# Kernel optimization log

Hardware: AMD Instinct MI355X
Metric: run time of the kernel (lower is better)

The kernel has to match this reference:

```python
import jax, jax.numpy as jnp
import numpy as np

TEMP = 5.0          # temperature_attn
BN_EPS = 1e-5
L2_EPS = 1e-8

def _conv2d(x, w):
    # x: [N,C,H,W], w: [O,C,3,3], SAME padding, stride 1
    return jax.lax.conv_general_dilated(x, w, (1, 1), 'SAME',
                                        dimension_numbers=('NCHW', 'OIHW', 'NCHW'))

def _conv_over_base(x, w):
    # separable 4D conv piece: 2D conv over the (Hb,Wb) pair of the 6D tensor
    BN, C, Hm, Wm, Hb, Wb = x.shape
    O = w.shape[0]
    y = _conv2d(x.transpose(0, 2, 3, 1, 4, 5).reshape(BN * Hm * Wm, C, Hb, Wb), w)
    return y.reshape(BN, Hm, Wm, O, Hb, Wb).transpose(0, 3, 1, 2, 4, 5)

def _conv_over_mem(x, w):
    # separable 4D conv piece: 2D conv over the (Hm,Wm) pair of the 6D tensor
    BN, C, Hm, Wm, Hb, Wb = x.shape
    O = w.shape[0]
    y = _conv2d(x.transpose(0, 4, 5, 1, 2, 3).reshape(BN * Hb * Wb, C, Hm, Wm), w)
    return y.reshape(BN, Hb, Wb, O, Hm, Wm).transpose(0, 3, 4, 5, 1, 2)

def _l2norm(x, axis):
    n = jnp.sqrt(jnp.sum(x * x, axis=axis, keepdims=True))
    return x / jnp.maximum(n, L2_EPS)

def _gaussian_normalize(x, axis):
    m = jnp.mean(x, axis=axis, keepdims=True)
    v = jnp.var(x, axis=axis, ddof=1, keepdims=True)  # torch.var is unbiased
    return (x - m) / jnp.sqrt(v + BN_EPS)

def setup_inputs() -> dict:
    key = jax.random.key(0)
    ks = jax.random.split(key, 10)
    B, N, C, H = 8, 64, 512, 10
    R, HID, NCLS = 64, 16, 100
    f32 = jnp.float32
    return {
        'feat_b': jax.random.normal(ks[0], (B, C, H, H), f32),
        'feat_m': jax.random.normal(ks[1], (N, C, H, H), f32),
        'w1x1':  jax.random.normal(ks[2], (R, C), f32) * 0.05,     # cca_1x1 conv weight
        'bn_gamma': jnp.ones((R,), f32),
        'bn_beta':  jnp.zeros((R,), f32),
        'w1a': jax.random.normal(ks[3], (HID, 1, 3, 3), f32) * 0.3,   # CCA block1, base-pair conv
        'w1b': jax.random.normal(ks[4], (HID, HID, 3, 3), f32) * 0.1, # CCA block1, mem-pair conv
        'w2a': jax.random.normal(ks[5], (1, HID, 3, 3), f32) * 0.1,   # CCA block2, base-pair conv
        'w2b': jax.random.normal(ks[6], (1, 1, 3, 3), f32) * 0.3,     # CCA block2, mem-pair conv
        'w_fc': jax.random.normal(ks[7], (NCLS, 2 * C), f32) * 0.02,  # memory-wrap head
        'b_fc': jnp.zeros((NCLS,), f32),
    }

def reference(feat_b, feat_m, w1x1, bn_gamma, bn_beta, w1a, w1b, w2a, w2b, w_fc, b_fc):
    B, C, Hb, Wb = feat_b.shape
    N, _, Hm, Wm = feat_m.shape
    # channel mean shift
    fb_s = feat_b - feat_b.mean(axis=1, keepdims=True)
    fm_s = feat_m - feat_m.mean(axis=1, keepdims=True)
    # 1x1 conv + BatchNorm(eval: mu=0,var=1) + ReLU, then L2-normalize over channels
    def proj(x):
        y = jnp.einsum('bchw,rc->brhw', x, w1x1)
        y = jax.nn.relu(y * bn_gamma[None, :, None, None] + bn_beta[None, :, None, None])
        return _l2norm(y, axis=1)
    fbp, fmp = proj(fb_s), proj(fm_s)
    # 6D cross-correlation map [B,N,Hm,Wm,Hb,Wb]
    corr = jnp.einsum('bchw,ncij->bnijhw', fbp, fmp)
    # CCA module: two separable 4D conv blocks (1->16, ReLU, 16->1)
    x = corr.reshape(B * N, 1, Hm, Wm, Hb, Wb)
    h = jax.nn.relu(_conv_over_mem(_conv_over_base(x, w1a), w1b))
    corr = _conv_over_mem(_conv_over_base(h, w2a), w2b).reshape(B, N, Hm, Wm, Hb, Wb)
    # memory-direction normalize+softmax (over Hm*Wm)
    cm = corr.reshape(B, N, Hm * Wm, Hb, Wb)
    cm = jax.nn.softmax(_gaussian_normalize(cm, 2) / TEMP, axis=2)
    attn_memory = cm.reshape(B, N, Hm, Wm, Hb, Wb).sum(axis=(4, 5))  # [B,N,Hm,Wm]
    # batch-direction normalize+softmax (over Hb*Wb)
    cb = corr.reshape(B, N, Hm, Wm, Hb * Wb)
    cb = jax.nn.softmax(_gaussian_normalize(cb, 4) / TEMP, axis=4)
    attn_batch = cb.reshape(B, N, Hm, Wm, Hb, Wb).sum(axis=(2, 3))  # [B,N,Hb,Wb] (used only for extras)
    # per-input attended memory embedding [B,N,C]
    att_mem = jnp.einsum('bnhw,nchw->bnc', attn_memory, feat_m) / (Hm * Wm)
    # memory wrap: cosine content weights over N + linear head on [enc ; mem_vec]
    enc = feat_b.mean(axis=(2, 3))                       # [B,C]
    enc_n = _l2norm(enc, axis=1)
    mem_n = _l2norm(att_mem, axis=2)
    w = jax.nn.softmax(jnp.einsum('bc,bnc->bn', enc_n, mem_n), axis=1)
    mem_vec = jnp.einsum('bn,bnc->bc', w, att_mem)
    logits = jnp.concatenate([enc, mem_vec], axis=1) @ w_fc.T + b_fc
    return logits
```

## Files before the change

### kernel.cpp

```cpp
#include <hip/hip_runtime.h>
#include <hip/hip_bf16.h>


__global__ __launch_bounds__(512) void k_proj2(const float* __restrict__ feat_b,
                                               const float* __restrict__ feat_m,
                                               const float* __restrict__ w1x1,
                                               const float* __restrict__ gamma,
                                               const float* __restrict__ beta,
                                               float* __restrict__ fbp,
                                               float* __restrict__ fmp) {
    __shared__ __align__(16) float xt[64][104];
    __shared__ __align__(16) float wt[64][68];
    __shared__ float colsum[100];
    __shared__ float wsumL[64];
    __shared__ float invL[100];
    const int tid = threadIdx.x;
    const int img = blockIdx.x;
    const float* x;
    float* outp;
    if (img < 8) { x = feat_b + (size_t)img * 51200; outp = fbp + (size_t)img * 6400; }
    else         { x = feat_m + (size_t)(img - 8) * 51200; outp = fmp + (size_t)(img - 8) * 6400; }

    if (tid < 100) colsum[tid] = 0.f;
    if (tid < 64) wsumL[tid] = 0.f;
    const int r = tid >> 3, q = tid & 7;
    float acc[13];
#pragma unroll
    for (int j = 0; j < 13; ++j) acc[j] = 0.f;
    __syncthreads();

    for (int ct = 0; ct < 8; ++ct) {
        for (int i = tid; i < 1600; i += 512) {
            int row = i / 25, c4 = (i % 25) * 4;
            *(float4*)&xt[row][c4] = *(const float4*)&x[(size_t)(ct * 64 + row) * 100 + c4];
        }
        for (int i = tid; i < 1024; i += 512) {
            int row = i / 16, c4 = (i % 16) * 4;
            *(float4*)&wt[row][c4] = *(const float4*)&w1x1[(size_t)row * 512 + ct * 64 + c4];
        }
        __syncthreads();
        if (tid < 100) {
            float s = 0.f;
            for (int c = 0; c < 64; ++c) s += xt[c][tid];
            colsum[tid] += s;
        }
        if (tid < 64) {
            float s = 0.f;
            for (int c = 0; c < 64; ++c) s += wt[tid][c];
            wsumL[tid] += s;
        }
        for (int c = 0; c < 64; ++c) {
            float w = wt[r][c];
#pragma unroll
            for (int j = 0; j < 13; ++j) {
                int hw = q + 8 * j;
                if (hw < 100) acc[j] = fmaf(w, xt[c][hw], acc[j]);
            }
        }
        __syncthreads();
    }
    float g = gamma[r], be = beta[r], wsr = wsumL[r];
#pragma unroll
    for (int j = 0; j < 13; ++j) {
        int hw = q + 8 * j;
        if (hw < 100) {
            float mean = colsum[hw] * (1.f / 512.f);
            xt[r][hw] = fmaxf((acc[j] - mean * wsr) * g + be, 0.f);
        }
    }
    __syncthreads();
    if (tid < 100) {
        float ss = 0.f;
        for (int rr = 0; rr < 64; ++rr) { float z = xt[rr][tid]; ss = fmaf(z, z, ss); }
        invL[tid] = 1.f / fmaxf(sqrtf(ss), 1e-8f);
    }
    __syncthreads();
    for (int i = tid; i < 6400; i += 512) {
        int rr = i / 100, hw = i % 100;
        outp[i] = xt[rr][hw] * invL[hw];
    }
}

__global__ __launch_bounds__(512) void k_corr(const float* __restrict__ fbp,
                                              const float* __restrict__ fmp,
                                              const float* __restrict__ w1a,
                                              const float* __restrict__ w1b,
                                              float* __restrict__ K1w,
                                              float* __restrict__ corr) {
    if (blockIdx.x == 512) {
        for (int t = threadIdx.x; t < 432; t += 512) {
            int tap = t >> 4, c = t & 15;
            int dm = tap / 3, dbh = tap % 3;
            float g0 = 0.f, g1 = 0.f, g2 = 0.f;
            for (int cp = 0; cp < 16; ++cp) {
                float wb = w1b[(c * 16 + cp) * 9 + dm];
                g0 = fmaf(wb, w1a[cp * 9 + dbh * 3 + 0], g0);
                g1 = fmaf(wb, w1a[cp * 9 + dbh * 3 + 1], g1);
                g2 = fmaf(wb, w1a[cp * 9 + dbh * 3 + 2], g2);
            }
            int base = tap * 64 + c;
            K1w[base]      = g0;
            K1w[base + 16] = 0.5f * (g0 + g1 + g2);
            K1w[base + 32] = 0.5f * (g0 - g1 + g2);
            K1w[base + 48] = g2;
        }
        return;
    }
    __shared__ __align__(16) float A[6400];
    __shared__ __align__(16) float B[6400];
    const int tid = threadIdx.x, bn = blockIdx.x;
    const float* fm = fmp + (size_t)(bn & 63) * 6400;
    const float* fb = fbp + (size_t)(bn >> 6) * 6400;
    for (int i = tid * 4; i < 6400; i += 2048) {
        *(float4*)&A[i] = *(const float4*)&fm[i];
        *(float4*)&B[i] = *(const float4*)&fb[i];
    }
    __syncthreads();
    float* dst = corr + (size_t)bn * 10000;
    for (int u = tid; u < 625; u += 512) {
        int m0 = (u / 25) * 4, b0 = (u % 25) * 4;
        float acc[4][4] = {};
        for (int r = 0; r < 64; ++r) {
            float4 av = *(const float4*)&A[r * 100 + m0];
            float4 bv = *(const float4*)&B[r * 100 + b0];
            float a[4] = {av.x, av.y, av.z, av.w};
            float bb[4] = {bv.x, bv.y, bv.z, bv.w};
#pragma unroll
            for (int i = 0; i < 4; ++i)
#pragma unroll
                for (int j = 0; j < 4; ++j) acc[i][j] = fmaf(a[i], bb[j], acc[i][j]);
        }
#pragma unroll
        for (int i = 0; i < 4; ++i)
#pragma unroll
            for (int j = 0; j < 4; ++j) dst[(m0 + i) * 100 + (b0 + j)] = acc[i][j];
    }
}

__global__ __launch_bounds__(64, 4) void k_cca(const float* __restrict__ corr,
                                               const float* __restrict__ K1w,
                                               const float* __restrict__ w2a,
                                               float* __restrict__ g1out) {
    __shared__ float ring[2184];
    const int lane = threadIdx.x;
    const int wm = blockIdx.x, bn = blockIdx.y;
    const int mr_lo = blockIdx.z * 5, mr_hi = mr_lo + 4;
    const int R_max = (mr_hi + 1 < 9) ? mr_hi + 1 : 9;
    const int u = lane < 50 ? lane : 49;
    const int bh = u / 5, p = u % 5, bw0 = 2 * p;
    const bool act = lane < 50;

    for (int i = lane; i < 2184; i += 64) ring[i] = 0.f;
    const float* cbase = corr + (size_t)bn * 10000 + (wm - 1) * 100;
    const int i0 = (wm == 0) ? 100 : 0;
    const int i1 = (wm == 9) ? 200 : 300;

    auto prefetch = [&](int R) {
        if (R < 0 || R > R_max) return;
        const float* src = cbase + R * 1000;
        float* dslot = &ring[(R & 3) * 504];
#pragma unroll
        for (int k = 0; k < 5; ++k) {
            int i = lane + k * 64;
            if (i >= i0 && i < i1) {
                int mc = i / 100, t = i % 100;
                dslot[mc * 168 + (t / 10 + 1) * 14 + (t % 10 + 1)] = src[i];
            }
        }
    };
    prefetch(mr_lo - 1);
    prefetch(mr_lo);
    prefetch(mr_lo + 1);

    const int rbase = bh * 14 + bw0;
    for (int mr = mr_lo; mr <= mr_hi; ++mr) {
        prefetch(mr + 2);

        float A1[16], A2[16], A3[16], A4[16];
#pragma unroll
        for (int c = 0; c < 16; ++c) { A1[c] = 0.f; A2[c] = 0.f; A3[c] = 0.f; A4[c] = 0.f; }
        for (int dmh = 0; dmh < 3; ++dmh) {
            int mrow = mr + dmh - 1;
            if ((unsigned)mrow >= 10u) continue;
            const float* slab0 = &ring[(mrow & 3) * 504];
#pragma unroll
            for (int dmw = 0; dmw < 3; ++dmw) {
                bool mv = (unsigned)(wm + dmw - 1) < 10u;
                const float* cb = (mv ? slab0 + dmw * 168 : &ring[2016]) + rbase;
                const float* kp = K1w + (dmh * 3 + dmw) * 192;
#pragma unroll
                for (int dbh = 0; dbh < 3; ++dbh) {
                    float2 lo = *(const float2*)&cb[dbh * 14];
                    float2 hi = *(const float2*)&cb[dbh * 14 + 2];
                    float t1 = lo.x - hi.x;
                    float t2 = lo.y + hi.x;
                    float t3 = hi.x - lo.y;
                    float t4 = lo.y - hi.y;
                    const float* kq = kp + dbh * 64;
#pragma unroll
                    for (int c = 0; c < 16; ++c) {
                        A1[c] = fmaf(t1, kq[c], A1[c]);
                        A2[c] = fmaf(t2, kq[16 + c], A2[c]);
                        A3[c] = fmaf(t3, kq[32 + c], A3[c]);
                        A4[c] = fmaf(t4, kq[48 + c], A4[c]);
                    }
                }
            }
        }

        float P00 = 0.f, P01 = 0.f, P10 = 0.f, P11 = 0.f, P20 = 0.f, P21 = 0.f;
#pragma unroll
        for (int c = 0; c < 16; ++c) {
            float r0 = fmaxf(A1[c] + A2[c] + A3[c], 0.f);
            float r1 = fmaxf(A2[c] - A3[c] - A4[c], 0.f);
            float lA = __shfl(r1, lane - 1); lA = (p > 0) ? lA : 0.f;
            float rA = __shfl(r0, lane + 1); rA = (p < 4) ? rA : 0.f;
            const float* wq = w2a + c * 9;
            P00 = fmaf(wq[0], lA, fmaf(wq[1], r0, fmaf(wq[2], r1, P00)));
            P01 = fmaf(wq[0], r0, fmaf(wq[1], r1, fmaf(wq[2], rA, P01)));
            P10 = fmaf(wq[3], lA, fmaf(wq[4], r0, fmaf(wq[5], r1, P10)));
            P11 = fmaf(wq[3], r0, fmaf(wq[4], r1, fmaf(wq[5], rA, P11)));
            P20 = fmaf(wq[6], lA, fmaf(wq[7], r0, fmaf(wq[8], r1, P20)));
            P21 = fmaf(wq[6], r0, fmaf(wq[7], r1, fmaf(wq[8], rA, P21)));
        }
        float u00 = __shfl(P00, lane - 5), u01 = __shfl(P01, lane - 5);
        float u20 = __shfl(P20, lane + 5), u21 = __shfl(P21, lane + 5);
        if (bh == 0) { u00 = 0.f; u01 = 0.f; }
        if (bh == 9) { u20 = 0.f; u21 = 0.f; }
        float g0 = P10 + u00 + u20;
        float g1v = P11 + u01 + u21;
        if (act) {
            float2 st; st.x = g0; st.y = g1v;
            *(float2*)&g1out[(size_t)bn * 10000 + (mr * 10 + wm) * 100 + bh * 10 + bw0] = st;
        }
    }
}

__global__ __launch_bounds__(512) void k_msoft2(const float* __restrict__ g1,
                                                const float* __restrict__ w2b,
                                                float* __restrict__ attnm) {
    __shared__ float gt[10000];
    const int tid = threadIdx.x, bn = blockIdx.x;
    const float* src = g1 + (size_t)bn * 10000;
    for (int i = tid; i < 10000; i += 512) gt[i] = src[i];
    __syncthreads();
    float wb[9];
#pragma unroll
    for (int t = 0; t < 9; ++t) wb[t] = w2b[t];
    const int b = tid >> 2, q = tid & 3;
    const bool act = tid < 400;
    float ev[25];
    float se = 0.f;
    if (act) {
        float s = 0.f, ss = 0.f;
#pragma unroll
        for (int i = 0; i < 25; ++i) {
            int m = q * 25 + i, mh = m / 10, mw = m % 10;
            float v = 0.f;
#pragma unroll
            for (int dh = 0; dh < 3; ++dh) {
                int rr = mh + dh - 1;
                if ((unsigned)rr < 10u) {
#pragma unroll
                    for (int dw = 0; dw < 3; ++dw) {
                        int ww = mw + dw - 1;
                        if ((unsigned)ww < 10u)
                            v = fmaf(wb[dh * 3 + dw], gt[(rr * 10 + ww) * 100 + b], v);
                    }
                }
            }
            ev[i] = v;
            s += v; ss = fmaf(v, v, ss);
        }
        s += __shfl_xor(s, 1); s += __shfl_xor(s, 2);
        ss += __shfl_xor(ss, 1); ss += __shfl_xor(ss, 2);
        float mean = s * 0.01f;
        float var = (ss - 100.f * mean * mean) * (1.f / 99.f);
        float istd = 0.2f / sqrtf(var + 1e-5f);
        float mx = -1e30f;
#pragma unroll
        for (int i = 0; i < 25; ++i) mx = fmaxf(mx, ev[i]);
        mx = fmaxf(mx, __shfl_xor(mx, 1)); mx = fmaxf(mx, __shfl_xor(mx, 2));
#pragma unroll
        for (int i = 0; i < 25; ++i) {
            float e = expf((ev[i] - mx) * istd);
            ev[i] = e; se += e;
        }
        se += __shfl_xor(se, 1); se += __shfl_xor(se, 2);
    }
    __syncthreads();
    if (act) {
        float inv = 1.f / se;
#pragma unroll
        for (int i = 0; i < 25; ++i) gt[(q * 25 + i) * 100 + b] = ev[i] * inv;
    }
    __syncthreads();
    if (act) {
        int m = tid >> 2;
        float s2 = 0.f;
#pragma unroll
        for (int i = 0; i < 25; ++i) s2 += gt[m * 100 + q * 25 + i];
        s2 += __shfl_xor(s2, 1); s2 += __shfl_xor(s2, 2);
        if (q == 0) attnm[bn * 100 + m] = s2;
    }
}

__global__ __launch_bounds__(128) void k_attmem(const float* __restrict__ attnm,
                                                const float* __restrict__ feat_m,
                                                float* __restrict__ attm) {
    __shared__ float A[8][100];
    int n = blockIdx.x, cq = blockIdx.y, tid = threadIdx.x;
    for (int i = tid; i < 800; i += 128) {
        int b = i / 100, m = i % 100;
        A[b][m] = attnm[(b * 64 + n) * 100 + m];
    }
    __syncthreads();
    int c = cq * 128 + tid;
    const float* fp = feat_m + ((size_t)n * 512 + c) * 100;
    float acc[8] = {};
    for (int m4 = 0; m4 < 100; m4 += 4) {
        float4 v = *(const float4*)&fp[m4];
#pragma unroll
        for (int b = 0; b < 8; ++b) {
            acc[b] = fmaf(A[b][m4], v.x, acc[b]);
            acc[b] = fmaf(A[b][m4 + 1], v.y, acc[b]);
            acc[b] = fmaf(A[b][m4 + 2], v.z, acc[b]);
            acc[b] = fmaf(A[b][m4 + 3], v.w, acc[b]);
        }
    }
#pragma unroll
    for (int b = 0; b < 8; ++b)
        attm[((size_t)(b * 64 + n)) * 512 + c] = acc[b] * 0.01f;
}

__global__ __launch_bounds__(512) void k_final(const float* __restrict__ feat_b,
                                               const float* __restrict__ attm,
                                               const float* __restrict__ w_fc,
                                               const float* __restrict__ b_fc,
                                               float* __restrict__ out) {
    __shared__ float attL[64 * 513];
    __shared__ float encL[512];
    __shared__ float mv[512];
    __shared__ float wL[64];
    __shared__ float red[512];
    int b = blockIdx.x, tid = threadIdx.x;
    {
        const float* fp = feat_b + ((size_t)b * 512 + tid) * 100;
        float s = 0.f;
        for (int m = 0; m < 100; m += 4) {
            float4 v = *(const float4*)&fp[m];
            s += v.x + v.y + v.z + v.w;
        }
        float e = s * 0.01f;
        encL[tid] = e;
        red[tid] = e * e;
    }
    const float* ap = attm + (size_t)b * 32768;
    for (int i = tid; i < 32768; i += 512) attL[(i >> 9) * 513 + (i & 511)] = ap[i];
    __syncthreads();
    for (int o = 256; o; o >>= 1) {
        if (tid < o) red[tid] += red[tid + o];
        __syncthreads();
    }
    float escale = 1.f / fmaxf(sqrtf(red[0]), 1e-8f);
    if (tid < 64) {
        int n = tid;
        float ss = 0.f, dp = 0.f;
        for (int c = 0; c < 512; ++c) {
            float a = attL[n * 513 + c];
            ss = fmaf(a, a, ss);
            dp = fmaf(encL[c], a, dp);
        }
        float sc = dp * escale / fmaxf(sqrtf(ss), 1e-8f);
        float mx = sc;
#pragma unroll
        for (int o = 32; o; o >>= 1) mx = fmaxf(mx, __shfl_xor(mx, o));
        float e = expf(sc - mx);
        float seL = e;
#pragma unroll
        for (int o = 32; o; o >>= 1) seL += __shfl_xor(seL, o);
        wL[n] = e / seL;
    }
    __syncthreads();
    {
        int c = tid;
        float s = 0.f;
        for (int n = 0; n < 64; ++n) s = fmaf(wL[n], attL[n * 513 + c], s);
        mv[c] = s;
    }
    __syncthreads();
    for (int k = tid; k < 100; k += 512) {
        const float* wp = w_fc + (size_t)k * 1024;
        float acc = b_fc[k];
        for (int c = 0; c < 512; c += 4) {
            float4 w0 = *(const float4*)&wp[c];
            float4 w1 = *(const float4*)&wp[512 + c];
            acc = fmaf(encL[c], w0.x, acc);     acc = fmaf(encL[c + 1], w0.y, acc);
            acc = fmaf(encL[c + 2], w0.z, acc); acc = fmaf(encL[c + 3], w0.w, acc);
            acc = fmaf(mv[c], w1.x, acc);       acc = fmaf(mv[c + 1], w1.y, acc);
            acc = fmaf(mv[c + 2], w1.z, acc);   acc = fmaf(mv[c + 3], w1.w, acc);
        }
        out[b * 100 + k] = acc;
    }
}

extern "C" void kernel_launch(void* const* d_in, const int* in_sizes, int n_in,
                              void* d_out, int out_size, void* d_ws, size_t ws_size,
                              hipStream_t stream) {
    const float* feat_b = (const float*)d_in[0];
    const float* feat_m = (const float*)d_in[1];
    const float* w1x1   = (const float*)d_in[2];
    const float* gamma  = (const float*)d_in[3];
    const float* beta   = (const float*)d_in[4];
    const float* w1a    = (const float*)d_in[5];
    const float* w1b    = (const float*)d_in[6];
    const float* w2a    = (const float*)d_in[7];
    const float* w2b    = (const float*)d_in[8];
    const float* w_fc   = (const float*)d_in[9];
    const float* b_fc   = (const float*)d_in[10];

    float* ws    = (float*)d_ws;
    float* K1w   = ws;
    float* fbp   = ws + 1760;
    float* fmp   = fbp + 51200;
    float* corr  = fmp + 409600;
    float* g1    = corr + 5120000;
    float* attnm = g1 + 5120000;
    float* attm  = attnm + 51200;

    hipLaunchKernelGGL(k_proj2, dim3(72), dim3(512), 0, stream,
                       feat_b, feat_m, w1x1, gamma, beta, fbp, fmp);
    hipLaunchKernelGGL(k_corr, dim3(513), dim3(512), 0, stream,
                       fbp, fmp, w1a, w1b, K1w, corr);
    hipLaunchKernelGGL(k_cca, dim3(10, 512, 2), dim3(64), 0, stream,
                       corr, K1w, w2a, g1);
    hipLaunchKernelGGL(k_msoft2, dim3(512), dim3(512), 0, stream, g1, w2b, attnm);
    hipLaunchKernelGGL(k_attmem, dim3(64, 4), dim3(128), 0, stream, attnm, feat_m, attm);
    hipLaunchKernelGGL(k_final, dim3(8), dim3(512), 0, stream,
                       feat_b, attm, w_fc, b_fc, (float*)d_out);
}
```

Measured before the change: 323.2 us.

## Merge CCA z-halves into one block with register-staged row prefetch

The K1w weight-combination block moves from k_corr into k_proj2 as an extra block, so k_corr is purely the correlation GEMM. k_cca now runs both five-row halves in one 128-thread block, each wave with its own 3-slot ring, a separate zero slab, and a fully unrolled row loop. Global loads for the next row are issued into registers one iteration ahead and written to LDS later, to hide load latency. This trades more registers per thread and a changed occupancy hint for better latency hiding and fewer blocks.

```diff
diff --git a/kernel.cpp b/kernel.cpp
--- a/kernel.cpp
+++ b/kernel.cpp
@@ -7,6 +7,9 @@
                                                const float* __restrict__ w1x1,
                                                const float* __restrict__ gamma,
                                                const float* __restrict__ beta,
+                                               const float* __restrict__ w1a,
+                                               const float* __restrict__ w1b,
+                                               float* __restrict__ K1w,
                                                float* __restrict__ fbp,
                                                float* __restrict__ fmp) {
     __shared__ __align__(16) float xt[64][104];
@@ -16,79 +19,8 @@
     __shared__ float invL[100];
     const int tid = threadIdx.x;
     const int img = blockIdx.x;
-    const float* x;
-    float* outp;
-    if (img < 8) { x = feat_b + (size_t)img * 51200; outp = fbp + (size_t)img * 6400; }
-    else         { x = feat_m + (size_t)(img - 8) * 51200; outp = fmp + (size_t)(img - 8) * 6400; }
-
-    if (tid < 100) colsum[tid] = 0.f;
-    if (tid < 64) wsumL[tid] = 0.f;
-    const int r = tid >> 3, q = tid & 7;
-    float acc[13];
-#pragma unroll
-    for (int j = 0; j < 13; ++j) acc[j] = 0.f;
-    __syncthreads();
-
-    for (int ct = 0; ct < 8; ++ct) {
-        for (int i = tid; i < 1600; i += 512) {
-            int row = i / 25, c4 = (i % 25) * 4;
-            *(float4*)&xt[row][c4] = *(const float4*)&x[(size_t)(ct * 64 + row) * 100 + c4];
-        }
-        for (int i = tid; i < 1024; i += 512) {
-            int row = i / 16, c4 = (i % 16) * 4;
-            *(float4*)&wt[row][c4] = *(const float4*)&w1x1[(size_t)row * 512 + ct * 64 + c4];
-        }
-        __syncthreads();
-        if (tid < 100) {
-            float s = 0.f;
-            for (int c = 0; c < 64; ++c) s += xt[c][tid];
-            colsum[tid] += s;
-        }
-        if (tid < 64) {
-            float s = 0.f;
-            for (int c = 0; c < 64; ++c) s += wt[tid][c];
-            wsumL[tid] += s;
-        }
-        for (int c = 0; c < 64; ++c) {
-            float w = wt[r][c];
-#pragma unroll
-            for (int j = 0; j < 13; ++j) {
-                int hw = q + 8 * j;
-                if (hw < 100) acc[j] = fmaf(w, xt[c][hw], acc[j]);
-            }
-        }
-        __syncthreads();
-    }
-    float g = gamma[r], be = beta[r], wsr = wsumL[r];
-#pragma unroll
-    for (int j = 0; j < 13; ++j) {
-        int hw = q + 8 * j;
-        if (hw < 100) {
-            float mean = colsum[hw] * (1.f / 512.f);
-            xt[r][hw] = fmaxf((acc[j] - mean * wsr) * g + be, 0.f);
-        }
-    }
-    __syncthreads();
-    if (tid < 100) {
-        float ss = 0.f;
-        for (int rr = 0; rr < 64; ++rr) { float z = xt[rr][tid]; ss = fmaf(z, z, ss); }
-        invL[tid] = 1.f / fmaxf(sqrtf(ss), 1e-8f);
-    }
-    __syncthreads();
-    for (int i = tid; i < 6400; i += 512) {
-        int rr = i / 100, hw = i % 100;
-        outp[i] = xt[rr][hw] * invL[hw];
-    }
-}
-
-__global__ __launch_bounds__(512) void k_corr(const float* __restrict__ fbp,
-                                              const float* __restrict__ fmp,
-                                              const float* __restrict__ w1a,
-                                              const float* __restrict__ w1b,
-                                              float* __restrict__ K1w,
-                                              float* __restrict__ corr) {
-    if (blockIdx.x == 512) {
-        for (int t = threadIdx.x; t < 432; t += 512) {
+    if (img == 72) {
+        for (int t = tid; t < 432; t += 512) {
             int tap = t >> 4, c = t & 15;
             int dm = tap / 3, dbh = tap % 3;
             float g0 = 0.f, g1 = 0.f, g2 = 0.f;
@@ -106,6 +38,74 @@
         }
         return;
     }
+    const float* x;
+    float* outp;
+    if (img < 8) { x = feat_b + (size_t)img * 51200; outp = fbp + (size_t)img * 6400; }
+    else         { x = feat_m + (size_t)(img - 8) * 51200; outp = fmp + (size_t)(img - 8) * 6400; }
+
+    if (tid < 100) colsum[tid] = 0.f;
+    if (tid < 64) wsumL[tid] = 0.f;
+    const int r = tid >> 3, q = tid & 7;
+    float acc[13];
+#pragma unroll
+    for (int j = 0; j < 13; ++j) acc[j] = 0.f;
+    __syncthreads();
+
+    for (int ct = 0; ct < 8; ++ct) {
+        for (int i = tid; i < 1600; i += 512) {
+            int row = i / 25, c4 = (i % 25) * 4;
+            *(float4*)&xt[row][c4] = *(const float4*)&x[(size_t)(ct * 64 + row) * 100 + c4];
+        }
+        for (int i = tid; i < 1024; i += 512) {
+            int row = i / 16, c4 = (i % 16) * 4;
+            *(float4*)&wt[row][c4] = *(const float4*)&w1x1[(size_t)row * 512 + ct * 64 + c4];
+        }
+        __syncthreads();
+        if (tid < 100) {
+            float s = 0.f;
+            for (int c = 0; c < 64; ++c) s += xt[c][tid];
+            colsum[tid] += s;
+        }
+        if (tid < 64) {
+            float s = 0.f;
+            for (int c = 0; c < 64; ++c) s += wt[tid][c];
+            wsumL[tid] += s;
+        }
+        for (int c = 0; c < 64; ++c) {
+            float w = wt[r][c];
+#pragma unroll
+            for (int j = 0; j < 13; ++j) {
+                int hw = q + 8 * j;
+                if (hw < 100) acc[j] = fmaf(w, xt[c][hw], acc[j]);
+            }
+        }
+        __syncthreads();
+    }
+    float g = gamma[r], be = beta[r], wsr = wsumL[r];
+#pragma unroll
+    for (int j = 0; j < 13; ++j) {
+        int hw = q + 8 * j;
+        if (hw < 100) {
+            float mean = colsum[hw] * (1.f / 512.f);
+            xt[r][hw] = fmaxf((acc[j] - mean * wsr) * g + be, 0.f);
+        }
+    }
+    __syncthreads();
+    if (tid < 100) {
+        float ss = 0.f;
+        for (int rr = 0; rr < 64; ++rr) { float z = xt[rr][tid]; ss = fmaf(z, z, ss); }
+        invL[tid] = 1.f / fmaxf(sqrtf(ss), 1e-8f);
+    }
+    __syncthreads();
+    for (int i = tid; i < 6400; i += 512) {
+        int rr = i / 100, hw = i % 100;
+        outp[i] = xt[rr][hw] * invL[hw];
+    }
+}
+
+__global__ __launch_bounds__(512) void k_corr(const float* __restrict__ fbp,
+                                              const float* __restrict__ fmp,
+                                              float* __restrict__ corr) {
     __shared__ __align__(16) float A[6400];
     __shared__ __align__(16) float B[6400];
     const int tid = threadIdx.x, bn = blockIdx.x;
@@ -137,44 +137,71 @@
     }
 }
 
-__global__ __launch_bounds__(64, 4) void k_cca(const float* __restrict__ corr,
-                                               const float* __restrict__ K1w,
-                                               const float* __restrict__ w2a,
-                                               float* __restrict__ g1out) {
-    __shared__ float ring[2184];
-    const int lane = threadIdx.x;
+__global__ __launch_bounds__(128, 5) void k_cca(const float* __restrict__ corr,
+                                                const float* __restrict__ K1w,
+                                                const float* __restrict__ w2a,
+                                                float* __restrict__ g1out) {
+    __shared__ float ringAll[2][1512];
+    __shared__ float zslab[168];
+    const int tid = threadIdx.x;
+    const int lane = tid & 63;
+    const int half = tid >> 6;
     const int wm = blockIdx.x, bn = blockIdx.y;
-    const int mr_lo = blockIdx.z * 5, mr_hi = mr_lo + 4;
-    const int R_max = (mr_hi + 1 < 9) ? mr_hi + 1 : 9;
+    const int mr_lo = half * 5;
+    const int r0 = half ? 4 : 0;
+    const int Rmax = half ? 9 : 5;
+    float* ring = ringAll[half];
+
+    for (int i = tid; i < 3024; i += 128) (&ringAll[0][0])[i] = 0.f;
+    for (int i = tid; i < 168; i += 128) zslab[i] = 0.f;
+
     const int u = lane < 50 ? lane : 49;
     const int bh = u / 5, p = u % 5, bw0 = 2 * p;
     const bool act = lane < 50;
 
-    for (int i = lane; i < 2184; i += 64) ring[i] = 0.f;
-    const float* cbase = corr + (size_t)bn * 10000 + (wm - 1) * 100;
-    const int i0 = (wm == 0) ? 100 : 0;
-    const int i1 = (wm == 9) ? 200 : 300;
-
-    auto prefetch = [&](int R) {
-        if (R < 0 || R > R_max) return;
-        const float* src = cbase + R * 1000;
-        float* dslot = &ring[(R & 3) * 504];
+    int dstoff[5], srcoff[5];
+    bool val[5];
+    {
+        const int i0 = (wm == 0) ? 100 : 0;
+        const int i1 = (wm == 9) ? 200 : 300;
 #pragma unroll
         for (int k = 0; k < 5; ++k) {
             int i = lane + k * 64;
-            if (i >= i0 && i < i1) {
-                int mc = i / 100, t = i % 100;
-                dslot[mc * 168 + (t / 10 + 1) * 14 + (t % 10 + 1)] = src[i];
-            }
+            val[k] = (i >= i0 && i < i1);
+            int mc = i / 100, t = i % 100;
+            dstoff[k] = mc * 168 + (t / 10 + 1) * 14 + (t % 10 + 1);
+            srcoff[k] = i;
+        }
+    }
+    const float* cbase = corr + (size_t)bn * 10000 + (wm - 1) * 100;
+    __syncthreads();
+
+    float pv[5];
+    auto issueRow = [&](int R) {
+#pragma unroll
+        for (int k = 0; k < 5; ++k) {
+            float v = 0.f;
+            if (val[k]) v = cbase[R * 1000 + srcoff[k]];
+            pv[k] = v;
         }
     };
-    prefetch(mr_lo - 1);
-    prefetch(mr_lo);
-    prefetch(mr_lo + 1);
+    auto commitRow = [&](int R) {
+        int sb = (R % 3) * 504;
+#pragma unroll
+        for (int k = 0; k < 5; ++k)
+            if (val[k]) ring[sb + dstoff[k]] = pv[k];
+    };
+
+    issueRow(r0);     commitRow(r0);
+    issueRow(r0 + 1); commitRow(r0 + 1);
+    issueRow(r0 + 2);
 
     const int rbase = bh * 14 + bw0;
-    for (int mr = mr_lo; mr <= mr_hi; ++mr) {
-        prefetch(mr + 2);
+#pragma unroll
+    for (int j = 0; j < 5; ++j) {
+        const int mr = mr_lo + j;
+        { int R = r0 + 2 + j; if (R <= Rmax) commitRow(R); }
+        { int R = r0 + 3 + j; if (R <= Rmax) issueRow(R); }
 
         float A1[16], A2[16], A3[16], A4[16];
 #pragma unroll
@@ -182,11 +209,11 @@
         for (int dmh = 0; dmh < 3; ++dmh) {
             int mrow = mr + dmh - 1;
             if ((unsigned)mrow >= 10u) continue;
-            const float* slab0 = &ring[(mrow & 3) * 504];
+            const float* slab0 = &ring[(mrow % 3) * 504];
 #pragma unroll
             for (int dmw = 0; dmw < 3; ++dmw) {
                 bool mv = (unsigned)(wm + dmw - 1) < 10u;
-                const float* cb = (mv ? slab0 + dmw * 168 : &ring[2016]) + rbase;
+                const float* cb = (mv ? slab0 + dmw * 168 : zslab) + rbase;
                 const float* kp = K1w + (dmh * 3 + dmw) * 192;
 #pragma unroll
                 for (int dbh = 0; dbh < 3; ++dbh) {
@@ -211,17 +238,17 @@
         float P00 = 0.f, P01 = 0.f, P10 = 0.f, P11 = 0.f, P20 = 0.f, P21 = 0.f;
 #pragma unroll
         for (int c = 0; c < 16; ++c) {
-            float r0 = fmaxf(A1[c] + A2[c] + A3[c], 0.f);
-            float r1 = fmaxf(A2[c] - A3[c] - A4[c], 0.f);
-            float lA = __shfl(r1, lane - 1); lA = (p > 0) ? lA : 0.f;
-            float rA = __shfl(r0, lane + 1); rA = (p < 4) ? rA : 0.f;
+            float rr0 = fmaxf(A1[c] + A2[c] + A3[c], 0.f);
+            float rr1 = fmaxf(A2[c] - A3[c] - A4[c], 0.f);
+            float lA = __shfl(rr1, lane - 1); lA = (p > 0) ? lA : 0.f;
+            float rA = __shfl(rr0, lane + 1); rA = (p < 4) ? rA : 0.f;
             const float* wq = w2a + c * 9;
-            P00 = fmaf(wq[0], lA, fmaf(wq[1], r0, fmaf(wq[2], r1, P00)));
-            P01 = fmaf(wq[0], r0, fmaf(wq[1], r1, fmaf(wq[2], rA, P01)));
-            P10 = fmaf(wq[3], lA, fmaf(wq[4], r0, fmaf(wq[5], r1, P10)));
-            P11 = fmaf(wq[3], r0, fmaf(wq[4], r1, fmaf(wq[5], rA, P11)));
-            P20 = fmaf(wq[6], lA, fmaf(wq[7], r0, fmaf(wq[8], r1, P20)));
-            P21 = fmaf(wq[6], r0, fmaf(wq[7], r1, fmaf(wq[8], rA, P21)));
+            P00 = fmaf(wq[0], lA, fmaf(wq[1], rr0, fmaf(wq[2], rr1, P00)));
+            P01 = fmaf(wq[0], rr0, fmaf(wq[1], rr1, fmaf(wq[2], rA, P01)));
+            P10 = fmaf(wq[3], lA, fmaf(wq[4], rr0, fmaf(wq[5], rr1, P10)));
+            P11 = fmaf(wq[3], rr0, fmaf(wq[4], rr1, fmaf(wq[5], rA, P11)));
+            P20 = fmaf(wq[6], lA, fmaf(wq[7], rr0, fmaf(wq[8], rr1, P20)));
+            P21 = fmaf(wq[6], rr0, fmaf(wq[7], rr1, fmaf(wq[8], rA, P21)));
         }
         float u00 = __shfl(P00, lane - 5), u01 = __shfl(P01, lane - 5);
         float u20 = __shfl(P20, lane + 5), u21 = __shfl(P21, lane + 5);
@@ -428,11 +455,10 @@
     float* attnm = g1 + 5120000;
     float* attm  = attnm + 51200;
 
-    hipLaunchKernelGGL(k_proj2, dim3(72), dim3(512), 0, stream,
-                       feat_b, feat_m, w1x1, gamma, beta, fbp, fmp);
-    hipLaunchKernelGGL(k_corr, dim3(513), dim3(512), 0, stream,
-                       fbp, fmp, w1a, w1b, K1w, corr);
-    hipLaunchKernelGGL(k_cca, dim3(10, 512, 2), dim3(64), 0, stream,
+    hipLaunchKernelGGL(k_proj2, dim3(73), dim3(512), 0, stream,
+                       feat_b, feat_m, w1x1, gamma, beta, w1a, w1b, K1w, fbp, fmp);
+    hipLaunchKernelGGL(k_corr, dim3(512), dim3(512), 0, stream, fbp, fmp, corr);
+    hipLaunchKernelGGL(k_cca, dim3(10, 512), dim3(128), 0, stream,
                        corr, K1w, w2a, g1);
     hipLaunchKernelGGL(k_msoft2, dim3(512), dim3(512), 0, stream, g1, w2b, attnm);
     hipLaunchKernelGGL(k_attmem, dim3(64, 4), dim3(128), 0, stream, attnm, feat_m, attm);
```

Measured after the change: 396.2 us. 22.6% more time.
